# Kernel tuning notes

Measured on AMD Instinct MI355X. Metric: run time of the kernel, lower is better.

The kernel has to match this reference:

```python
import jax, jax.numpy as jnp
import numpy as np
import math

B, N, D, O, H = 8, 1024, 512, 512, 8
HD = O // H  # head_dim = 64


def setup_inputs() -> dict:
    key = jax.random.key(0)
    ks = jax.random.split(key, 12)
    x = jax.random.normal(ks[0], (B, N, D), dtype=jnp.float32)
    adj = jax.random.uniform(ks[1], (B, N, N), dtype=jnp.float32)  # unused by forward math
    mask = jax.random.randint(ks[2], (B, N), 0, 2) > 0  # bool padding mask
    # learned params (torch nn.Linear: y = x @ W.T + b)
    qkv_w = jax.random.normal(ks[3], (3 * O, D), dtype=jnp.float32) / math.sqrt(D)
    qkv_b = jnp.zeros((3 * O,), dtype=jnp.float32)
    # self_loop_W: 1/head_dim + U(0,1), per head, non-trainable
    self_loop_W = (1.0 / HD + jax.random.uniform(ks[4], (1, H, 1, 1))).astype(jnp.float32)
    w1 = jax.random.normal(ks[5], (O, O), dtype=jnp.float32) / math.sqrt(O)
    b1 = jnp.zeros((O,), dtype=jnp.float32)
    w2 = jax.random.normal(ks[6], (O, O), dtype=jnp.float32) / math.sqrt(O)
    b2 = jnp.zeros((O,), dtype=jnp.float32)
    wr = jax.random.normal(ks[7], (O, D), dtype=jnp.float32) / math.sqrt(D)
    br = jnp.zeros((O,), dtype=jnp.float32)
    return {"x": x, "adj": adj, "mask": mask, "self_loop_W": self_loop_W,
            "qkv_w": qkv_w, "qkv_b": qkv_b, "w1": w1, "b1": b1,
            "w2": w2, "b2": b2, "wr": wr, "br": br}


def reference(x, adj, mask, self_loop_W, qkv_w, qkv_b, w1, b1, w2, b2, wr, br):
    fmask = mask.astype(x.dtype)  # [B,N]
    # --- MoireAttention ---
    qkv = x @ qkv_w.T + qkv_b                       # [B,N,3O]
    qkv = qkv.reshape(B, N, 3, H, HD).transpose(2, 0, 3, 1, 4)  # [3,B,H,N,hd]
    Q, K, V = qkv[0], qkv[1], qkv[2]
    scores = jnp.einsum('bhnd,bhmd->bhnm', Q, K) / math.sqrt(HD)  # [B,H,N,N]
    eye = jnp.eye(N, dtype=scores.dtype)
    scores = scores + eye[None, None] * self_loop_W  # per-head diagonal self-loop bias
    mask2d = mask[:, None, :, None] & mask[:, None, None, :]  # [B,1,N,N]
    scores = jnp.where(mask2d, scores, jnp.asarray(-1e6, scores.dtype))
    attn = jax.nn.softmax(scores, axis=-1)
    h = jnp.einsum('bhnm,bhmd->bhnd', attn, V)      # [B,H,N,hd]
    h = h.transpose(0, 2, 1, 3).reshape(B, N, O)
    # --- mask, FFN (eval mode: noise/dropout are identity), mask ---
    h = h * fmask[..., None]
    h = jax.nn.relu(h @ w1.T + b1) @ w2.T + b2
    h = h * fmask[..., None]
    # --- residual blend ---
    x_proj = x @ wr.T + br
    return h * 0.5 + x_proj * 0.5
```

## Files before the change

kernel.cpp:

```cpp
#include <hip/hip_runtime.h>
#include <hip/hip_bf16.h>

typedef __attribute__((ext_vector_type(8))) short short8;
typedef __attribute__((ext_vector_type(4))) float f32x4;
typedef __attribute__((ext_vector_type(4))) short short4v;

#define BB 8
#define NN 1024
#define DD 512
#define OO 512
#define HH 8
#define HD 64
#define MM (BB * NN)

#define QSC 0.18033688f
#define KSHIFT -11.54156032f
#define KMASKED -30000.0f

__device__ __forceinline__ void gload_lds16(const void* g, void* l) {
  __builtin_amdgcn_global_load_lds(
      (const __attribute__((address_space(1))) void*)g,
      (__attribute__((address_space(3))) void*)l, 16, 0, 0);
}

#define SEG_N 10
struct ConvArgs {
  const float* src[SEG_N];
  __hip_bfloat16* dst[SEG_N];
  int n4[SEG_N];
};

__global__ void convert_kernel(ConvArgs a) {
  const int t = blockIdx.y;
  const int n4 = a.n4[t];
  const float4* fs = (const float4*)a.src[t];
  short4v* d = (short4v*)a.dst[t];
  for (int i = blockIdx.x * blockDim.x + threadIdx.x; i < n4;
       i += gridDim.x * blockDim.x) {
    const float4 v = fs[i];
    union { short4v s; __hip_bfloat16 h[4]; } u;
    u.h[0] = __float2bfloat16(v.x);
    u.h[1] = __float2bfloat16(v.y);
    u.h[2] = __float2bfloat16(v.z);
    u.h[3] = __float2bfloat16(v.w);
    d[i] = u.s;
  }
}

__global__ __launch_bounds__(256) void gemm_qkv(
    const __hip_bfloat16* __restrict__ A0, const __hip_bfloat16* __restrict__ B0,
    const __hip_bfloat16* __restrict__ bias0,
    __hip_bfloat16* __restrict__ out0, __hip_bfloat16* __restrict__ out1,
    __hip_bfloat16* __restrict__ out2, int Kd) {
  __shared__ __align__(16) __hip_bfloat16 smem[8192];
  __hip_bfloat16* As = smem;
  __hip_bfloat16* Bs = smem + 4096;

  const int tid  = threadIdx.x;
  const int wave = tid >> 6;
  const int lane = tid & 63;
  const int fl   = lane & 15;
  const int fk   = (lane >> 4) * 8;
  const int wm   = (wave & 1) * 64;
  const int wn   = (wave >> 1) * 64;
  const int m0   = blockIdx.y * 128;
  const int n0   = blockIdx.x * 128;
  const int glr  = lane >> 2;
  const int glc  = (lane & 3) * 8;

  f32x4 acc[4][4];
#pragma unroll
  for (int i = 0; i < 4; ++i)
#pragma unroll
    for (int j = 0; j < 4; ++j) acc[i][j] = (f32x4){0.f, 0.f, 0.f, 0.f};

  char* lb = (char*)smem;
  for (int k0 = 0; k0 < Kd; k0 += 32) {
    __syncthreads();
    gload_lds16(A0 + (size_t)(m0 + wave * 16 + glr) * Kd + k0 + glc,
                lb + wave * 1024 + lane * 16);
    gload_lds16(A0 + (size_t)(m0 + 64 + wave * 16 + glr) * Kd + k0 + glc,
                lb + (wave + 4) * 1024 + lane * 16);
    gload_lds16(B0 + (size_t)(n0 + wave * 16 + glr) * Kd + k0 + glc,
                lb + 8192 + wave * 1024 + lane * 16);
    gload_lds16(B0 + (size_t)(n0 + 64 + wave * 16 + glr) * Kd + k0 + glc,
                lb + 8192 + (wave + 4) * 1024 + lane * 16);
    __syncthreads();

    short8 af[4], bfr[4];
#pragma unroll
    for (int i = 0; i < 4; ++i)
      af[i] = *(const short8*)&As[(wm + i * 16 + fl) * 32 + fk];
#pragma unroll
    for (int j = 0; j < 4; ++j)
      bfr[j] = *(const short8*)&Bs[(wn + j * 16 + fl) * 32 + fk];
#pragma unroll
    for (int i = 0; i < 4; ++i)
#pragma unroll
      for (int j = 0; j < 4; ++j)
        acc[i][j] = __builtin_amdgcn_mfma_f32_16x16x32_bf16(af[i], bfr[j],
                                                            acc[i][j], 0, 0, 0);
  }

  const int rb = (lane >> 4) * 4;
  const int part = n0 >> 9;
  if (part < 2) {
    __hip_bfloat16* dst = (part == 0) ? out0 : out1;
    const float sc = (part == 0) ? QSC : 1.0f;
#pragma unroll
    for (int j = 0; j < 4; ++j) {
      const int colb  = n0 + wn + j * 16;
      const int o     = colb & 511;
      const int headq = o >> 6;
      const int d     = (o & 63) + fl;
      const float bi  = __bfloat162float(bias0[colb + fl]);
#pragma unroll
      for (int i = 0; i < 4; ++i) {
#pragma unroll
        for (int r = 0; r < 4; ++r) {
          const int row = m0 + wm + i * 16 + rb + r;
          const int bb  = row >> 10;
          const int nn  = row & 1023;
          dst[((size_t)((bb << 3) + headq) * NN + nn) * HD + d] =
              __float2bfloat16((acc[i][j][r] + bi) * sc);
        }
      }
    }
  } else {
    __syncthreads();
    __hip_bfloat16* tsc = smem + wave * 1120;
    const int bb  = (m0 + wm) >> 10;
    const int nnb = (m0 + wm) & 1023;
    const int dl  = lane >> 2;
    const int cc  = (lane & 3) * 16;
#pragma unroll
    for (int j = 0; j < 4; ++j) {
      const int colb  = n0 + wn + j * 16;
      const int o     = colb & 511;
      const int headq = o >> 6;
      const int dbase = o & 63;
      const float bi  = __bfloat162float(bias0[colb + fl]);
#pragma unroll
      for (int i = 0; i < 4; ++i) {
#pragma unroll
        for (int r = 0; r < 4; ++r) {
          const int rr = i * 16 + rb + r;
          tsc[fl * 70 + rr] = __float2bfloat16(acc[i][j][r] + bi);
        }
      }
      uint4 r0 = *(const uint4*)&tsc[dl * 70 + cc];
      uint4 r1 = *(const uint4*)&tsc[dl * 70 + cc + 8];
      __hip_bfloat16* vdst =
          out2 + ((size_t)((bb << 3) + headq) * HD + dbase + dl) * NN + nnb;
      *(uint4*)&vdst[cc] = r0;
      *(uint4*)&vdst[cc + 8] = r1;
    }
  }
}

template <int MODE>
__global__ __launch_bounds__(256) void gemm64(
    const __hip_bfloat16* __restrict__ A0, const __hip_bfloat16* __restrict__ B0,
    const __hip_bfloat16* __restrict__ A1, const __hip_bfloat16* __restrict__ B1,
    const __hip_bfloat16* __restrict__ bias0, const __hip_bfloat16* __restrict__ bias1,
    const int* __restrict__ mask,
    __hip_bfloat16* __restrict__ out0, float* __restrict__ outf,
    int N, int Kd) {
  __shared__ __align__(16) __hip_bfloat16 smem[4096];
  __hip_bfloat16* As = smem;
  __hip_bfloat16* Bs = smem + 2048;

  const int tid  = threadIdx.x;
  const int wave = tid >> 6;
  const int lane = tid & 63;
  const int fl   = lane & 15;
  const int fk   = (lane >> 4) * 8;
  const int wm   = (wave & 1) * 32;
  const int wn   = (wave >> 1) * 32;
  const int m0   = blockIdx.y * 64;
  const int n0   = blockIdx.x * 64;
  const int glr  = lane >> 2;
  const int glc  = (lane & 3) * 8;

  f32x4 acc[2][2];
#pragma unroll
  for (int i = 0; i < 2; ++i)
#pragma unroll
    for (int j = 0; j < 2; ++j) acc[i][j] = (f32x4){0.f, 0.f, 0.f, 0.f};

  char* lb = (char*)smem;
  const int npairs = (MODE == 2) ? 2 : 1;
  for (int p = 0; p < npairs; ++p) {
    const __hip_bfloat16* Ap = (p == 0) ? A0 : A1;
    const __hip_bfloat16* Bp = (p == 0) ? B0 : B1;
    for (int k0 = 0; k0 < Kd; k0 += 32) {
      __syncthreads();
      gload_lds16(Ap + (size_t)(m0 + wave * 16 + glr) * Kd + k0 + glc,
                  lb + wave * 1024 + lane * 16);
      gload_lds16(Bp + (size_t)(n0 + wave * 16 + glr) * Kd + k0 + glc,
                  lb + 4096 + wave * 1024 + lane * 16);
      __syncthreads();

      short8 af[2], bfr[2];
#pragma unroll
      for (int i = 0; i < 2; ++i)
        af[i] = *(const short8*)&As[(wm + i * 16 + fl) * 32 + fk];
#pragma unroll
      for (int j = 0; j < 2; ++j)
        bfr[j] = *(const short8*)&Bs[(wn + j * 16 + fl) * 32 + fk];
#pragma unroll
      for (int i = 0; i < 2; ++i)
#pragma unroll
        for (int j = 0; j < 2; ++j)
          acc[i][j] = __builtin_amdgcn_mfma_f32_16x16x32_bf16(af[i], bfr[j],
                                                              acc[i][j], 0, 0, 0);
    }
  }

  const int rb = (lane >> 4) * 4;
  if (MODE == 1) {
#pragma unroll
    for (int j = 0; j < 2; ++j) {
      const int col  = n0 + wn + j * 16 + fl;
      const float bi = __bfloat162float(bias0[col]);
#pragma unroll
      for (int i = 0; i < 2; ++i) {
#pragma unroll
        for (int r = 0; r < 4; ++r) {
          const int row = m0 + wm + i * 16 + rb + r;
          float v = fmaxf(acc[i][j][r] + bi, 0.f);
          if (mask[row] == 0) v = 0.f;
          out0[(size_t)row * N + col] = __float2bfloat16(v);
        }
      }
    }
  } else {
#pragma unroll
    for (int j = 0; j < 2; ++j) {
      const int col   = n0 + wn + j * 16 + fl;
      const float b2v = __bfloat162float(bias0[col]);
      const float brv = __bfloat162float(bias1[col]);
#pragma unroll
      for (int i = 0; i < 2; ++i) {
#pragma unroll
        for (int r = 0; r < 4; ++r) {
          const int row = m0 + wm + i * 16 + rb + r;
          const float v = acc[i][j][r] + brv + (mask[row] != 0 ? b2v : 0.f);
          outf[(size_t)row * N + col] = 0.5f * v;
        }
      }
    }
  }
}

__global__ __launch_bounds__(512) void attn_kernel(
    const __hip_bfloat16* __restrict__ Qb, const __hip_bfloat16* __restrict__ Kb,
    const __hip_bfloat16* __restrict__ Vt, const __hip_bfloat16* __restrict__ slw,
    const int* __restrict__ mask, __hip_bfloat16* __restrict__ hb) {
  __shared__ __hip_bfloat16 Qs[128 * 72];
  __shared__ __hip_bfloat16 Ks[64 * 72];
  __shared__ __hip_bfloat16 Vs[64 * 72];
  __shared__ __hip_bfloat16 Ps[128 * 72];
  __shared__ float Msf[NN];

  const int tid  = threadIdx.x;
  const int wave = tid >> 6;
  const int lane = tid & 63;
  const int fl   = lane & 15;
  const int quad = lane >> 4;
  const int fk   = quad * 8;
  const int rb   = quad * 4;
  const int bh   = blockIdx.x & 63;
  const int qblk = blockIdx.x >> 6;
  const int b    = bh >> 3;
  const int head = bh & 7;
  const int q0   = qblk * 128;

  const float slwL2 = __bfloat162float(slw[head]) * 1.44269504f;

  {
    const int srow = tid >> 2;
    const int sc   = (tid & 3) * 16;
    const __hip_bfloat16* qg = Qb + ((size_t)bh * NN + q0) * HD;
    uint4 v0 = *(const uint4*)(qg + srow * HD + sc);
    uint4 v1 = *(const uint4*)(qg + srow * HD + sc + 8);
    *(uint4*)&Qs[srow * 72 + sc] = v0;
    *(uint4*)&Qs[srow * 72 + sc + 8] = v1;
#pragma unroll
    for (int k = 0; k < 2; ++k) {
      const int idx = tid * 2 + k;
      Msf[idx] = (mask[b * NN + idx] != 0) ? KSHIFT : KMASKED;
    }
  }
  __syncthreads();
  const short8 qa0 = *(const short8*)&Qs[(wave * 16 + fl) * 72 + fk];
  const short8 qa1 = *(const short8*)&Qs[(wave * 16 + fl) * 72 + fk + 32];

  const int srow2 = tid >> 3;
  const int sc2   = (tid & 7) * 8;

  float lsum = 0.f;
  f32x4 Oacc[4];
#pragma unroll
  for (int t = 0; t < 4; ++t) Oacc[t] = (f32x4){0.f, 0.f, 0.f, 0.f};

  const int kbdiag = 2 * qblk + (wave >> 2);

  for (int kb = 0; kb < NN / 64; ++kb) {
    const int kbase = kb * 64;
    __syncthreads();
    {
      const __hip_bfloat16* kg = Kb + ((size_t)bh * NN + kbase) * HD;
      uint4 v0 = *(const uint4*)(kg + srow2 * HD + sc2);
      *(uint4*)&Ks[srow2 * 72 + sc2] = v0;
      const __hip_bfloat16* vg = Vt + ((size_t)bh * HD + srow2) * NN + kbase;
      uint4 w0 = *(const uint4*)(vg + sc2);
      *(uint4*)&Vs[srow2 * 72 + sc2] = w0;
    }
    __syncthreads();

    f32x4 sfr[4];
#pragma unroll
    for (int j = 0; j < 4; ++j) {
      const short8 kf0 = *(const short8*)&Ks[(j * 16 + fl) * 72 + fk];
      const short8 kf1 = *(const short8*)&Ks[(j * 16 + fl) * 72 + fk + 32];
      f32x4 z = (f32x4){0.f, 0.f, 0.f, 0.f};
      z = __builtin_amdgcn_mfma_f32_16x16x32_bf16(kf0, qa0, z, 0, 0, 0);
      z = __builtin_amdgcn_mfma_f32_16x16x32_bf16(kf1, qa1, z, 0, 0, 0);
      sfr[j] = z;
    }

    if (kb == kbdiag) {
      if ((fl >> 2) == quad) sfr[wave & 3][fl & 3] += slwL2;
    }

#pragma unroll
    for (int j = 0; j < 4; ++j) {
      const f32x4 mb4 = *(const f32x4*)&Msf[kbase + j * 16 + quad * 4];
      union { short4v s; __hip_bfloat16 h[4]; } pu;
      float ps = 0.f;
#pragma unroll
      for (int e = 0; e < 4; ++e) {
        const float pv = exp2f(sfr[j][e] + mb4[e]);
        ps += pv;
        pu.h[e] = __float2bfloat16(pv);
      }
      lsum += ps;
      *(short4v*)&Ps[(wave * 16 + fl) * 72 + j * 16 + quad * 4] = pu.s;
    }

    const short8 pa0 = *(const short8*)&Ps[(wave * 16 + fl) * 72 + fk];
    const short8 pa1 = *(const short8*)&Ps[(wave * 16 + fl) * 72 + fk + 32];
#pragma unroll
    for (int t = 0; t < 4; ++t) {
      const short8 vf0 = *(const short8*)&Vs[(t * 16 + fl) * 72 + fk];
      const short8 vf1 = *(const short8*)&Vs[(t * 16 + fl) * 72 + fk + 32];
      Oacc[t] = __builtin_amdgcn_mfma_f32_16x16x32_bf16(pa0, vf0, Oacc[t], 0, 0, 0);
      Oacc[t] = __builtin_amdgcn_mfma_f32_16x16x32_bf16(pa1, vf1, Oacc[t], 0, 0, 0);
    }
  }

  float l = lsum;
  l += __shfl_xor(l, 16, 64);
  l += __shfl_xor(l, 32, 64);
  const int qrow_me = q0 + wave * 16 + fl;
  const float qm = (mask[b * NN + qrow_me] != 0) ? 1.f : 0.f;
  const float sf = qm / fmaxf(l, 1e-30f);

  float scl[4];
#pragma unroll
  for (int r = 0; r < 4; ++r) scl[r] = __shfl(sf, rb + r, 64);

#pragma unroll
  for (int t = 0; t < 4; ++t) {
    const int d = t * 16 + fl;
#pragma unroll
    for (int r = 0; r < 4; ++r) {
      const int qrow_g = q0 + wave * 16 + rb + r;
      hb[(size_t)(b * NN + qrow_g) * OO + head * HD + d] =
          __float2bfloat16(Oacc[t][r] * scl[r]);
    }
  }
}

extern "C" void kernel_launch(void* const* d_in, const int* in_sizes, int n_in,
                              void* d_out, int out_size, void* d_ws, size_t ws_size,
                              hipStream_t stream) {
  const float* x_raw    = (const float*)d_in[0];
  const int* mask       = (const int*)d_in[2];
  const float* slw_raw  = (const float*)d_in[3];
  const float* qkvw_raw = (const float*)d_in[4];
  const float* qkvb_raw = (const float*)d_in[5];
  const float* w1_raw   = (const float*)d_in[6];
  const float* b1_raw   = (const float*)d_in[7];
  const float* w2_raw   = (const float*)d_in[8];
  const float* b2_raw   = (const float*)d_in[9];
  const float* wr_raw   = (const float*)d_in[10];
  const float* br_raw   = (const float*)d_in[11];
  float* outf           = (float*)d_out;

  __hip_bfloat16* p = (__hip_bfloat16*)d_ws;
  __hip_bfloat16* xc    = p; p += (size_t)MM * DD;
  __hip_bfloat16* qkvwc = p; p += 3 * OO * DD;
  __hip_bfloat16* w1c   = p; p += OO * OO;
  __hip_bfloat16* w2c   = p; p += OO * OO;
  __hip_bfloat16* wrc   = p; p += OO * DD;
  __hip_bfloat16* qkvbc = p; p += 3 * OO;
  __hip_bfloat16* b1c   = p; p += OO;
  __hip_bfloat16* b2c   = p; p += OO;
  __hip_bfloat16* brc   = p; p += OO;
  __hip_bfloat16* slwc  = p; p += 64;
  const size_t ebuf = (size_t)BB * HH * NN * HD;
  __hip_bfloat16* Qb = p; p += ebuf;
  __hip_bfloat16* Kb = p; p += ebuf;
  __hip_bfloat16* Vb = p; p += ebuf;
  __hip_bfloat16* hb = (__hip_bfloat16*)d_out;
  __hip_bfloat16* tb = Kb;

  if (ws_size < (size_t)((char*)p - (char*)d_ws)) return;

  ConvArgs ca;
  ca.src[0] = x_raw;    ca.dst[0] = xc;    ca.n4[0] = MM * DD / 4;
  ca.src[1] = qkvw_raw; ca.dst[1] = qkvwc; ca.n4[1] = 3 * OO * DD / 4;
  ca.src[2] = w1_raw;   ca.dst[2] = w1c;   ca.n4[2] = OO * OO / 4;
  ca.src[3] = w2_raw;   ca.dst[3] = w2c;   ca.n4[3] = OO * OO / 4;
  ca.src[4] = wr_raw;   ca.dst[4] = wrc;   ca.n4[4] = OO * DD / 4;
  ca.src[5] = qkvb_raw; ca.dst[5] = qkvbc; ca.n4[5] = 3 * OO / 4;
  ca.src[6] = b1_raw;   ca.dst[6] = b1c;   ca.n4[6] = OO / 4;
  ca.src[7] = b2_raw;   ca.dst[7] = b2c;   ca.n4[7] = OO / 4;
  ca.src[8] = br_raw;   ca.dst[8] = brc;   ca.n4[8] = OO / 4;
  ca.src[9] = slw_raw;  ca.dst[9] = slwc;  ca.n4[9] = HH / 4;
  convert_kernel<<<dim3(128, SEG_N), 256, 0, stream>>>(ca);

  gemm_qkv<<<dim3(3 * OO / 128, MM / 128), 256, 0, stream>>>(
      xc, qkvwc, qkvbc, Qb, Kb, Vb, DD);
  attn_kernel<<<BB * HH * (NN / 128), 512, 0, stream>>>(Qb, Kb, Vb, slwc, mask, hb);
  gemm64<1><<<dim3(OO / 64, MM / 64), 256, 0, stream>>>(
      hb, w1c, nullptr, nullptr, b1c, nullptr, mask, tb, nullptr, OO, OO);
  gemm64<2><<<dim3(OO / 64, MM / 64), 256, 0, stream>>>(
      tb, w2c, xc, wrc, b2c, brc, mask, nullptr, outf, OO, DD);
}
```

Before: 226.9 us.

## Fuse FFN and residual GEMMs into one kernel; convert x in-GEMM

```diff
diff --git a/kernel.cpp b/kernel.cpp
--- a/kernel.cpp
+++ b/kernel.cpp
@@ -23,7 +23,16 @@
       (__attribute__((address_space(3))) void*)l, 16, 0, 0);
 }
 
-#define SEG_N 10
+__device__ __forceinline__ uint2 cvt4(float4 v) {
+  union { uint2 u; __hip_bfloat16 h[4]; } t;
+  t.h[0] = __float2bfloat16(v.x);
+  t.h[1] = __float2bfloat16(v.y);
+  t.h[2] = __float2bfloat16(v.z);
+  t.h[3] = __float2bfloat16(v.w);
+  return t.u;
+}
+
+#define SEG_N 9
 struct ConvArgs {
   const float* src[SEG_N];
   __hip_bfloat16* dst[SEG_N];
@@ -34,21 +43,14 @@
   const int t = blockIdx.y;
   const int n4 = a.n4[t];
   const float4* fs = (const float4*)a.src[t];
-  short4v* d = (short4v*)a.dst[t];
+  uint2* d = (uint2*)a.dst[t];
   for (int i = blockIdx.x * blockDim.x + threadIdx.x; i < n4;
-       i += gridDim.x * blockDim.x) {
-    const float4 v = fs[i];
-    union { short4v s; __hip_bfloat16 h[4]; } u;
-    u.h[0] = __float2bfloat16(v.x);
-    u.h[1] = __float2bfloat16(v.y);
-    u.h[2] = __float2bfloat16(v.z);
-    u.h[3] = __float2bfloat16(v.w);
-    d[i] = u.s;
-  }
+       i += gridDim.x * blockDim.x)
+    d[i] = cvt4(fs[i]);
 }
 
 __global__ __launch_bounds__(256) void gemm_qkv(
-    const __hip_bfloat16* __restrict__ A0, const __hip_bfloat16* __restrict__ B0,
+    const float* __restrict__ A0f, const __hip_bfloat16* __restrict__ B0,
     const __hip_bfloat16* __restrict__ bias0,
     __hip_bfloat16* __restrict__ out0, __hip_bfloat16* __restrict__ out1,
     __hip_bfloat16* __restrict__ out2, int Kd) {
@@ -67,6 +69,8 @@
   const int n0   = blockIdx.x * 128;
   const int glr  = lane >> 2;
   const int glc  = (lane & 3) * 8;
+  const int sr   = tid >> 3;
+  const int sc   = (tid & 7) * 4;
 
   f32x4 acc[4][4];
 #pragma unroll
@@ -77,10 +81,12 @@
   char* lb = (char*)smem;
   for (int k0 = 0; k0 < Kd; k0 += 32) {
     __syncthreads();
-    gload_lds16(A0 + (size_t)(m0 + wave * 16 + glr) * Kd + k0 + glc,
-                lb + wave * 1024 + lane * 16);
-    gload_lds16(A0 + (size_t)(m0 + 64 + wave * 16 + glr) * Kd + k0 + glc,
-                lb + (wave + 4) * 1024 + lane * 16);
+#pragma unroll
+    for (int rnd = 0; rnd < 4; ++rnd) {
+      const int row = rnd * 32 + sr;
+      float4 v = *(const float4*)(A0f + (size_t)(m0 + row) * Kd + k0 + sc);
+      *(uint2*)&As[row * 32 + sc] = cvt4(v);
+    }
     gload_lds16(B0 + (size_t)(n0 + wave * 16 + glr) * Kd + k0 + glc,
                 lb + 8192 + wave * 1024 + lane * 16);
     gload_lds16(B0 + (size_t)(n0 + 64 + wave * 16 + glr) * Kd + k0 + glc,
@@ -106,7 +112,7 @@
   const int part = n0 >> 9;
   if (part < 2) {
     __hip_bfloat16* dst = (part == 0) ? out0 : out1;
-    const float sc = (part == 0) ? QSC : 1.0f;
+    const float scf = (part == 0) ? QSC : 1.0f;
 #pragma unroll
     for (int j = 0; j < 4; ++j) {
       const int colb  = n0 + wn + j * 16;
@@ -122,7 +128,7 @@
           const int bb  = row >> 10;
           const int nn  = row & 1023;
           dst[((size_t)((bb << 3) + headq) * NN + nn) * HD + d] =
-              __float2bfloat16((acc[i][j][r] + bi) * sc);
+              __float2bfloat16((acc[i][j][r] + bi) * scf);
         }
       }
     }
@@ -158,96 +164,129 @@
   }
 }
 
-template <int MODE>
-__global__ __launch_bounds__(256) void gemm64(
-    const __hip_bfloat16* __restrict__ A0, const __hip_bfloat16* __restrict__ B0,
-    const __hip_bfloat16* __restrict__ A1, const __hip_bfloat16* __restrict__ B1,
-    const __hip_bfloat16* __restrict__ bias0, const __hip_bfloat16* __restrict__ bias1,
-    const int* __restrict__ mask,
-    __hip_bfloat16* __restrict__ out0, float* __restrict__ outf,
-    int N, int Kd) {
-  __shared__ __align__(16) __hip_bfloat16 smem[4096];
-  __hip_bfloat16* As = smem;
-  __hip_bfloat16* Bs = smem + 2048;
+__global__ __launch_bounds__(256) void ffn_fused(
+    const __hip_bfloat16* __restrict__ hb, const float* __restrict__ xf,
+    const __hip_bfloat16* __restrict__ w1c, const __hip_bfloat16* __restrict__ w2c,
+    const __hip_bfloat16* __restrict__ wrc, const __hip_bfloat16* __restrict__ b1c,
+    const __hip_bfloat16* __restrict__ b2c, const __hip_bfloat16* __restrict__ brc,
+    const int* __restrict__ mask, float* __restrict__ outf) {
+  __shared__ __align__(16) __hip_bfloat16 Ts[32 * 520];
+  __shared__ __align__(16) __hip_bfloat16 Asm[32 * 32];
+  __shared__ __align__(16) __hip_bfloat16 Bsm[512 * 32];
 
   const int tid  = threadIdx.x;
   const int wave = tid >> 6;
   const int lane = tid & 63;
   const int fl   = lane & 15;
-  const int fk   = (lane >> 4) * 8;
-  const int wm   = (wave & 1) * 32;
-  const int wn   = (wave >> 1) * 32;
-  const int m0   = blockIdx.y * 64;
-  const int n0   = blockIdx.x * 64;
+  const int quad = lane >> 4;
+  const int fk   = quad * 8;
+  const int rb   = quad * 4;
+  const int m0   = blockIdx.x * 32;
+  const int sr   = tid >> 3;
+  const int sc   = (tid & 7) * 4;
   const int glr  = lane >> 2;
   const int glc  = (lane & 3) * 8;
 
-  f32x4 acc[2][2];
+  f32x4 acc[2][8];
 #pragma unroll
   for (int i = 0; i < 2; ++i)
 #pragma unroll
-    for (int j = 0; j < 2; ++j) acc[i][j] = (f32x4){0.f, 0.f, 0.f, 0.f};
-
-  char* lb = (char*)smem;
-  const int npairs = (MODE == 2) ? 2 : 1;
-  for (int p = 0; p < npairs; ++p) {
-    const __hip_bfloat16* Ap = (p == 0) ? A0 : A1;
-    const __hip_bfloat16* Bp = (p == 0) ? B0 : B1;
-    for (int k0 = 0; k0 < Kd; k0 += 32) {
-      __syncthreads();
-      gload_lds16(Ap + (size_t)(m0 + wave * 16 + glr) * Kd + k0 + glc,
-                  lb + wave * 1024 + lane * 16);
-      gload_lds16(Bp + (size_t)(n0 + wave * 16 + glr) * Kd + k0 + glc,
-                  lb + 4096 + wave * 1024 + lane * 16);
-      __syncthreads();
-
-      short8 af[2], bfr[2];
-#pragma unroll
-      for (int i = 0; i < 2; ++i)
-        af[i] = *(const short8*)&As[(wm + i * 16 + fl) * 32 + fk];
-#pragma unroll
-      for (int j = 0; j < 2; ++j)
-        bfr[j] = *(const short8*)&Bs[(wn + j * 16 + fl) * 32 + fk];
-#pragma unroll
-      for (int i = 0; i < 2; ++i)
-#pragma unroll
-        for (int j = 0; j < 2; ++j)
-          acc[i][j] = __builtin_amdgcn_mfma_f32_16x16x32_bf16(af[i], bfr[j],
-                                                              acc[i][j], 0, 0, 0);
-    }
-  }
-
-  const int rb = (lane >> 4) * 4;
-  if (MODE == 1) {
-#pragma unroll
-    for (int j = 0; j < 2; ++j) {
-      const int col  = n0 + wn + j * 16 + fl;
-      const float bi = __bfloat162float(bias0[col]);
-#pragma unroll
-      for (int i = 0; i < 2; ++i) {
-#pragma unroll
-        for (int r = 0; r < 4; ++r) {
-          const int row = m0 + wm + i * 16 + rb + r;
-          float v = fmaxf(acc[i][j][r] + bi, 0.f);
-          if (mask[row] == 0) v = 0.f;
-          out0[(size_t)row * N + col] = __float2bfloat16(v);
-        }
+    for (int j = 0; j < 8; ++j) acc[i][j] = (f32x4){0.f, 0.f, 0.f, 0.f};
+
+  for (int k0 = 0; k0 < OO; k0 += 32) {
+    __syncthreads();
+    {
+      uint2 v = *(const uint2*)(hb + (size_t)(m0 + sr) * OO + k0 + sc);
+      *(uint2*)&Asm[sr * 32 + sc] = v;
+    }
+#pragma unroll
+    for (int c = 0; c < 8; ++c)
+      gload_lds16(w1c + (size_t)(wave * 128 + c * 16 + glr) * OO + k0 + glc,
+                  (char*)Bsm + wave * 8192 + c * 1024 + lane * 16);
+    __syncthreads();
+
+    short8 af0 = *(const short8*)&Asm[fl * 32 + fk];
+    short8 af1 = *(const short8*)&Asm[(16 + fl) * 32 + fk];
+#pragma unroll
+    for (int j = 0; j < 8; ++j) {
+      const short8 bfr = *(const short8*)&Bsm[(wave * 128 + j * 16 + fl) * 32 + fk];
+      acc[0][j] = __builtin_amdgcn_mfma_f32_16x16x32_bf16(af0, bfr, acc[0][j], 0, 0, 0);
+      acc[1][j] = __builtin_amdgcn_mfma_f32_16x16x32_bf16(af1, bfr, acc[1][j], 0, 0, 0);
+    }
+  }
+#pragma unroll
+  for (int j = 0; j < 8; ++j) {
+    const int col  = wave * 128 + j * 16 + fl;
+    const float bi = __bfloat162float(b1c[col]);
+#pragma unroll
+    for (int i = 0; i < 2; ++i) {
+#pragma unroll
+      for (int r = 0; r < 4; ++r) {
+        const int row = i * 16 + rb + r;
+        float v = fmaxf(acc[i][j][r] + bi, 0.f);
+        if (mask[m0 + row] == 0) v = 0.f;
+        Ts[row * 520 + col] = __float2bfloat16(v);
       }
     }
-  } else {
-#pragma unroll
-    for (int j = 0; j < 2; ++j) {
-      const int col   = n0 + wn + j * 16 + fl;
-      const float b2v = __bfloat162float(bias0[col]);
-      const float brv = __bfloat162float(bias1[col]);
-#pragma unroll
-      for (int i = 0; i < 2; ++i) {
-#pragma unroll
-        for (int r = 0; r < 4; ++r) {
-          const int row = m0 + wm + i * 16 + rb + r;
-          const float v = acc[i][j][r] + brv + (mask[row] != 0 ? b2v : 0.f);
-          outf[(size_t)row * N + col] = 0.5f * v;
-        }
+  }
+#pragma unroll
+  for (int i = 0; i < 2; ++i)
+#pragma unroll
+    for (int j = 0; j < 8; ++j) acc[i][j] = (f32x4){0.f, 0.f, 0.f, 0.f};
+  __syncthreads();
+
+  for (int k0 = 0; k0 < OO; k0 += 32) {
+    __syncthreads();
+#pragma unroll
+    for (int c = 0; c < 8; ++c)
+      gload_lds16(w2c + (size_t)(wave * 128 + c * 16 + glr) * OO + k0 + glc,
+                  (char*)Bsm + wave * 8192 + c * 1024 + lane * 16);
+    __syncthreads();
+
+    short8 af0 = *(const short8*)&Ts[fl * 520 + k0 + fk];
+    short8 af1 = *(const short8*)&Ts[(16 + fl) * 520 + k0 + fk];
+#pragma unroll
+    for (int j = 0; j < 8; ++j) {
+      const short8 bfr = *(const short8*)&Bsm[(wave * 128 + j * 16 + fl) * 32 + fk];
+      acc[0][j] = __builtin_amdgcn_mfma_f32_16x16x32_bf16(af0, bfr, acc[0][j], 0, 0, 0);
+      acc[1][j] = __builtin_amdgcn_mfma_f32_16x16x32_bf16(af1, bfr, acc[1][j], 0, 0, 0);
+    }
+  }
+
+  for (int k0 = 0; k0 < DD; k0 += 32) {
+    __syncthreads();
+    {
+      float4 v = *(const float4*)(xf + (size_t)(m0 + sr) * DD + k0 + sc);
+      *(uint2*)&Asm[sr * 32 + sc] = cvt4(v);
+    }
+#pragma unroll
+    for (int c = 0; c < 8; ++c)
+      gload_lds16(wrc + (size_t)(wave * 128 + c * 16 + glr) * DD + k0 + glc,
+                  (char*)Bsm + wave * 8192 + c * 1024 + lane * 16);
+    __syncthreads();
+
+    short8 af0 = *(const short8*)&Asm[fl * 32 + fk];
+    short8 af1 = *(const short8*)&Asm[(16 + fl) * 32 + fk];
+#pragma unroll
+    for (int j = 0; j < 8; ++j) {
+      const short8 bfr = *(const short8*)&Bsm[(wave * 128 + j * 16 + fl) * 32 + fk];
+      acc[0][j] = __builtin_amdgcn_mfma_f32_16x16x32_bf16(af0, bfr, acc[0][j], 0, 0, 0);
+      acc[1][j] = __builtin_amdgcn_mfma_f32_16x16x32_bf16(af1, bfr, acc[1][j], 0, 0, 0);
+    }
+  }
+
+#pragma unroll
+  for (int j = 0; j < 8; ++j) {
+    const int col   = wave * 128 + j * 16 + fl;
+    const float b2v = __bfloat162float(b2c[col]);
+    const float brv = __bfloat162float(brc[col]);
+#pragma unroll
+    for (int i = 0; i < 2; ++i) {
+#pragma unroll
+      for (int r = 0; r < 4; ++r) {
+        const int row = m0 + i * 16 + rb + r;
+        const float v = acc[i][j][r] + brv + (mask[row] != 0 ? b2v : 0.f);
+        outf[(size_t)row * OO + col] = 0.5f * v;
       }
     }
   }
@@ -400,7 +439,6 @@
   float* outf           = (float*)d_out;
 
   __hip_bfloat16* p = (__hip_bfloat16*)d_ws;
-  __hip_bfloat16* xc    = p; p += (size_t)MM * DD;
   __hip_bfloat16* qkvwc = p; p += 3 * OO * DD;
   __hip_bfloat16* w1c   = p; p += OO * OO;
   __hip_bfloat16* w2c   = p; p += OO * OO;
@@ -414,29 +452,25 @@
   __hip_bfloat16* Qb = p; p += ebuf;
   __hip_bfloat16* Kb = p; p += ebuf;
   __hip_bfloat16* Vb = p; p += ebuf;
-  __hip_bfloat16* hb = (__hip_bfloat16*)d_out;
-  __hip_bfloat16* tb = Kb;
+  __hip_bfloat16* hb = p; p += ebuf;
 
   if (ws_size < (size_t)((char*)p - (char*)d_ws)) return;
 
   ConvArgs ca;
-  ca.src[0] = x_raw;    ca.dst[0] = xc;    ca.n4[0] = MM * DD / 4;
-  ca.src[1] = qkvw_raw; ca.dst[1] = qkvwc; ca.n4[1] = 3 * OO * DD / 4;
-  ca.src[2] = w1_raw;   ca.dst[2] = w1c;   ca.n4[2] = OO * OO / 4;
-  ca.src[3] = w2_raw;   ca.dst[3] = w2c;   ca.n4[3] = OO * OO / 4;
-  ca.src[4] = wr_raw;   ca.dst[4] = wrc;   ca.n4[4] = OO * DD / 4;
-  ca.src[5] = qkvb_raw; ca.dst[5] = qkvbc; ca.n4[5] = 3 * OO / 4;
-  ca.src[6] = b1_raw;   ca.dst[6] = b1c;   ca.n4[6] = OO / 4;
-  ca.src[7] = b2_raw;   ca.dst[7] = b2c;   ca.n4[7] = OO / 4;
-  ca.src[8] = br_raw;   ca.dst[8] = brc;   ca.n4[8] = OO / 4;
-  ca.src[9] = slw_raw;  ca.dst[9] = slwc;  ca.n4[9] = HH / 4;
-  convert_kernel<<<dim3(128, SEG_N), 256, 0, stream>>>(ca);
+  ca.src[0] = qkvw_raw; ca.dst[0] = qkvwc; ca.n4[0] = 3 * OO * DD / 4;
+  ca.src[1] = w1_raw;   ca.dst[1] = w1c;   ca.n4[1] = OO * OO / 4;
+  ca.src[2] = w2_raw;   ca.dst[2] = w2c;   ca.n4[2] = OO * OO / 4;
+  ca.src[3] = wr_raw;   ca.dst[3] = wrc;   ca.n4[3] = OO * DD / 4;
+  ca.src[4] = qkvb_raw; ca.dst[4] = qkvbc; ca.n4[4] = 3 * OO / 4;
+  ca.src[5] = b1_raw;   ca.dst[5] = b1c;   ca.n4[5] = OO / 4;
+  ca.src[6] = b2_raw;   ca.dst[6] = b2c;   ca.n4[6] = OO / 4;
+  ca.src[7] = br_raw;   ca.dst[7] = brc;   ca.n4[7] = OO / 4;
+  ca.src[8] = slw_raw;  ca.dst[8] = slwc;  ca.n4[8] = HH / 4;
+  convert_kernel<<<dim3(64, SEG_N), 256, 0, stream>>>(ca);
 
   gemm_qkv<<<dim3(3 * OO / 128, MM / 128), 256, 0, stream>>>(
-      xc, qkvwc, qkvbc, Qb, Kb, Vb, DD);
+      x_raw, qkvwc, qkvbc, Qb, Kb, Vb, DD);
   attn_kernel<<<BB * HH * (NN / 128), 512, 0, stream>>>(Qb, Kb, Vb, slwc, mask, hb);
-  gemm64<1><<<dim3(OO / 64, MM / 64), 256, 0, stream>>>(
-      hb, w1c, nullptr, nullptr, b1c, nullptr, mask, tb, nullptr, OO, OO);
-  gemm64<2><<<dim3(OO / 64, MM / 64), 256, 0, stream>>>(
-      tb, w2c, xc, wrc, b2c, brc, mask, nullptr, outf, OO, DD);
-}
+  ffn_fused<<<MM / 32, 256, 0, stream>>>(hb, x_raw, w1c, w2c, wrc, b1c, b2c,
+                                         brc, mask, outf);
+}
```

New measurement: 245.4 us. +8.1%, slower.
